# Performance work log

Hardware: AMD Instinct MI355X
Metric: run time of the kernel (lower is better)

## Reference

```python
import jax, jax.numpy as jnp
import numpy as np

N_NODES = 100000
N_EDGES = 1600000
D_FEAT = 64


def setup_inputs() -> dict:
    key = jax.random.key(0)
    k1, k2, k3 = jax.random.split(key, 3)
    adj_indices = jax.random.randint(k1, (2, N_EDGES), 0, N_NODES, dtype=jnp.int64 if jax.config.jax_enable_x64 else jnp.int32)
    # symmetric-normalized-like edge weights in (0, 1)
    adj_values = jax.random.uniform(k2, (N_EDGES,), dtype=jnp.float32)
    feats = jax.random.normal(k3, (N_NODES, D_FEAT), dtype=jnp.float32)
    return {"adj_indices": adj_indices, "adj_values": adj_values, "feats": feats}


def reference(adj_indices, adj_values, feats):
    """out = sparse_adj @ feats  (COO SpMM via gather + segment_sum).

    adj_indices: [2, E] int (row, col) coordinates of nonzeros
    adj_values : [E] float nonzero values
    feats      : [N, d] dense node features
    returns    : [N, d]
    """
    rows = adj_indices[0]
    cols = adj_indices[1]
    # gather neighbor features, scale by edge weight: [E, d]
    msgs = adj_values[:, None] * feats[cols]
    # scatter-add into destination rows: [N, d]
    return jax.ops.segment_sum(msgs, rows, num_segments=feats.shape[0])
```

## Files before the change

### kernel.cpp

```cpp
#include <hip/hip_runtime.h>

#define NN 100000
#define NE 1600000
#define DF 64
#define RPB 32
#define NBS 3328
#define NBU 3125
#define OFS_STRIDE (NBS + 1)
#define CHK 4096
#define SCAP 768
#define SPB 13

__device__ inline float bflo(unsigned int u) { return __uint_as_float(u << 16); }
__device__ inline float bfhi(unsigned int u) { return __uint_as_float(u & 0xFFFF0000u); }

__device__ inline unsigned int bfpack(float lo, float hi) {
    unsigned int ul = __float_as_uint(lo), uh = __float_as_uint(hi);
    ul = (ul + 0x7FFFu + ((ul >> 16) & 1u)) >> 16;
    uh = (uh + 0x7FFFu + ((uh >> 16) & 1u)) & 0xFFFF0000u;
    return ul | uh;
}

__global__ __launch_bounds__(256) void cvt_kernel(const float* __restrict__ feats,
                                                  uint4* __restrict__ fbf) {
    int t = blockIdx.x * blockDim.x + threadIdx.x;
    if (t >= NN * DF / 8) return;
    const float4* f4 = reinterpret_cast<const float4*>(feats);
    float4 a = f4[2 * t];
    float4 b = f4[2 * t + 1];
    uint4 o;
    o.x = bfpack(a.x, a.y);
    o.y = bfpack(a.z, a.w);
    o.z = bfpack(b.x, b.y);
    o.w = bfpack(b.z, b.w);
    fbf[t] = o;
}

__global__ __launch_bounds__(256) void part_kernel(
    const int* __restrict__ rows, const int* __restrict__ cols,
    const float* __restrict__ vals, unsigned short* __restrict__ ofs,
    int2* __restrict__ packed, int E)
{
    int c = blockIdx.x;
    int base = c * CHK;
    int n = E - base; if (n > CHK) n = CHK;
    int t = threadIdx.x;

    __shared__ int cnt[NBS];
    __shared__ int cnt2[NBS];
    __shared__ int scanv[NBS];
    __shared__ int tsum[256];

    for (int b = t; b < NBS; b += 256) { cnt[b] = 0; cnt2[b] = 0; }
    __syncthreads();

    int rr[16]; int cc[16]; float vv[16];
#pragma unroll
    for (int k = 0; k < 16; ++k) {
        int i = t + k * 256;
        if (i < n) {
            rr[k] = rows[base + i];
            cc[k] = cols[base + i];
            vv[k] = vals[base + i];
            atomicAdd(&cnt[rr[k] >> 5], 1);
        }
    }
    __syncthreads();

    int local[SPB]; int s = 0;
#pragma unroll
    for (int j = 0; j < SPB; ++j) { local[j] = cnt[t * SPB + j]; s += local[j]; }
    tsum[t] = s;
    __syncthreads();
    for (int d = 1; d < 256; d <<= 1) {
        int x = (t >= d) ? tsum[t - d] : 0;
        __syncthreads();
        tsum[t] += x;
        __syncthreads();
    }
    int run = tsum[t] - s;
#pragma unroll
    for (int j = 0; j < SPB; ++j) { scanv[t * SPB + j] = run; run += local[j]; }
    __syncthreads();

    unsigned short* og = ofs + (size_t)c * OFS_STRIDE;
    for (int b = t; b < NBS; b += 256) og[b] = (unsigned short)scanv[b];
    if (t == 0) og[NBS] = (unsigned short)n;

#pragma unroll
    for (int k = 0; k < 16; ++k) {
        int i = t + k * 256;
        if (i < n) {
            int r = rr[k];
            int b = r >> 5;
            int rank = atomicAdd(&cnt2[b], 1);
            int pos = base + scanv[b] + rank;
            packed[pos] = make_int2(cc[k] | ((r & 31) << 17), __float_as_int(vv[k]));
        }
    }
}

__global__ __launch_bounds__(256) void spmm_kernel(
    const unsigned short* __restrict__ ofs, const int2* __restrict__ packed,
    const unsigned short* __restrict__ fbf, float* __restrict__ out, int nc)
{
    int b = blockIdx.x;
    int t = threadIdx.x;

    __shared__ int2 sorted[SCAP];
    __shared__ int cnt[RPB];
    __shared__ int rstart[RPB + 1];

    if (t < RPB) cnt[t] = 0;
    __syncthreads();

    int c2 = t + 256;
    int sA = 0, eA = 0, sB = 0, eB = 0;
    if (t < nc) {
        const unsigned short* og = ofs + (size_t)t * OFS_STRIDE + b;
        sA = og[0]; eA = og[1];
    }
    if (c2 < nc) {
        const unsigned short* og = ofs + (size_t)c2 * OFS_STRIDE + b;
        sB = og[0]; eB = og[1];
    }
    int lenA = eA - sA, lenB = eB - sB;

    int2 ebA[8], ebB[8];
#pragma unroll
    for (int k = 0; k < 8; ++k) if (k < lenA) ebA[k] = packed[t * CHK + sA + k];
#pragma unroll
    for (int k = 0; k < 8; ++k) if (k < lenB) ebB[k] = packed[c2 * CHK + sB + k];

#pragma unroll
    for (int k = 0; k < 8; ++k) if (k < lenA) atomicAdd(&cnt[(ebA[k].x >> 17) & 31], 1);
    for (int i = sA + 8; i < eA; ++i) atomicAdd(&cnt[(packed[t * CHK + i].x >> 17) & 31], 1);
#pragma unroll
    for (int k = 0; k < 8; ++k) if (k < lenB) atomicAdd(&cnt[(ebB[k].x >> 17) & 31], 1);
    for (int i = sB + 8; i < eB; ++i) atomicAdd(&cnt[(packed[c2 * CHK + i].x >> 17) & 31], 1);
    __syncthreads();

    if (t < RPB) {
        int v = cnt[t];
        int incl = v;
        for (int d = 1; d < RPB; d <<= 1) {
            int x = __shfl_up(incl, d, 64);
            if (t >= d) incl += x;
        }
        rstart[t] = incl - v;
        if (t == RPB - 1) rstart[RPB] = incl;
    }
    __syncthreads();
    if (t < RPB) cnt[t] = rstart[t];
    __syncthreads();

#pragma unroll
    for (int k = 0; k < 8; ++k) if (k < lenA) {
        int rl = (ebA[k].x >> 17) & 31;
        int pos = atomicAdd(&cnt[rl], 1);
        if (pos < SCAP) sorted[pos] = make_int2(ebA[k].x & 0x1FFFF, ebA[k].y);
    }
    for (int i = sA + 8; i < eA; ++i) {
        int2 cv = packed[t * CHK + i];
        int rl = (cv.x >> 17) & 31;
        int pos = atomicAdd(&cnt[rl], 1);
        if (pos < SCAP) sorted[pos] = make_int2(cv.x & 0x1FFFF, cv.y);
    }
#pragma unroll
    for (int k = 0; k < 8; ++k) if (k < lenB) {
        int rl = (ebB[k].x >> 17) & 31;
        int pos = atomicAdd(&cnt[rl], 1);
        if (pos < SCAP) sorted[pos] = make_int2(ebB[k].x & 0x1FFFF, ebB[k].y);
    }
    for (int i = sB + 8; i < eB; ++i) {
        int2 cv = packed[c2 * CHK + i];
        int rl = (cv.x >> 17) & 31;
        int pos = atomicAdd(&cnt[rl], 1);
        if (pos < SCAP) sorted[pos] = make_int2(cv.x & 0x1FFFF, cv.y);
    }
    __syncthreads();

    int w = t >> 6;
    int lane = t & 63;
    int grp = lane >> 4;
    int fq = lane & 15;
    int rowbase = b * RPB;

    for (int rl = w * 8; rl < w * 8 + 8; ++rl) {
        int row = rowbase + rl;
        int beg = rstart[rl], end = rstart[rl + 1];
        float4 acc = make_float4(0.f, 0.f, 0.f, 0.f);
        int i = beg + grp;
        for (; i + 12 < end; i += 16) {
            int2 e0 = sorted[i];
            int2 e1 = sorted[i + 4];
            int2 e2 = sorted[i + 8];
            int2 e3 = sorted[i + 12];
            const uint2 g0 = *reinterpret_cast<const uint2*>(fbf + (size_t)e0.x * DF + fq * 4);
            const uint2 g1 = *reinterpret_cast<const uint2*>(fbf + (size_t)e1.x * DF + fq * 4);
            const uint2 g2 = *reinterpret_cast<const uint2*>(fbf + (size_t)e2.x * DF + fq * 4);
            const uint2 g3 = *reinterpret_cast<const uint2*>(fbf + (size_t)e3.x * DF + fq * 4);
            float v0 = __int_as_float(e0.y), v1 = __int_as_float(e1.y);
            float v2 = __int_as_float(e2.y), v3 = __int_as_float(e3.y);
            acc.x += v0 * bflo(g0.x); acc.y += v0 * bfhi(g0.x);
            acc.z += v0 * bflo(g0.y); acc.w += v0 * bfhi(g0.y);
            acc.x += v1 * bflo(g1.x); acc.y += v1 * bfhi(g1.x);
            acc.z += v1 * bflo(g1.y); acc.w += v1 * bfhi(g1.y);
            acc.x += v2 * bflo(g2.x); acc.y += v2 * bfhi(g2.x);
            acc.z += v2 * bflo(g2.y); acc.w += v2 * bfhi(g2.y);
            acc.x += v3 * bflo(g3.x); acc.y += v3 * bfhi(g3.x);
            acc.z += v3 * bflo(g3.y); acc.w += v3 * bfhi(g3.y);
        }
        for (; i + 4 < end; i += 8) {
            int2 e0 = sorted[i];
            int2 e1 = sorted[i + 4];
            const uint2 g0 = *reinterpret_cast<const uint2*>(fbf + (size_t)e0.x * DF + fq * 4);
            const uint2 g1 = *reinterpret_cast<const uint2*>(fbf + (size_t)e1.x * DF + fq * 4);
            float v0 = __int_as_float(e0.y), v1 = __int_as_float(e1.y);
            acc.x += v0 * bflo(g0.x); acc.y += v0 * bfhi(g0.x);
            acc.z += v0 * bflo(g0.y); acc.w += v0 * bfhi(g0.y);
            acc.x += v1 * bflo(g1.x); acc.y += v1 * bfhi(g1.x);
            acc.z += v1 * bflo(g1.y); acc.w += v1 * bfhi(g1.y);
        }
        if (i < end) {
            int2 e0 = sorted[i];
            const uint2 g0 = *reinterpret_cast<const uint2*>(fbf + (size_t)e0.x * DF + fq * 4);
            float v0 = __int_as_float(e0.y);
            acc.x += v0 * bflo(g0.x); acc.y += v0 * bfhi(g0.x);
            acc.z += v0 * bflo(g0.y); acc.w += v0 * bfhi(g0.y);
        }
#pragma unroll
        for (int m = 16; m <= 32; m <<= 1) {
            acc.x += __shfl_xor(acc.x, m, 64);
            acc.y += __shfl_xor(acc.y, m, 64);
            acc.z += __shfl_xor(acc.z, m, 64);
            acc.w += __shfl_xor(acc.w, m, 64);
        }
        if (grp == 0 && row < NN)
            *reinterpret_cast<float4*>(out + (size_t)row * DF + fq * 4) = acc;
    }
}


extern "C" void kernel_launch(void* const* d_in, const int* in_sizes, int n_in,
                              void* d_out, int out_size, void* d_ws, size_t ws_size,
                              hipStream_t stream) {
    const int* adj_indices = (const int*)d_in[0];
    const float* adj_values = (const float*)d_in[1];
    const float* feats = (const float*)d_in[2];
    float* out = (float*)d_out;

    const int E = in_sizes[1];
    const int* rows = adj_indices;
    const int* cols = adj_indices + E;

    const int nc = (E + CHK - 1) / CHK;

    unsigned short* fbf = (unsigned short*)d_ws;
    size_t fbf_bytes = (size_t)NN * DF * 2;
    unsigned short* ofs = (unsigned short*)((char*)d_ws + fbf_bytes);
    size_t ofs_bytes = (size_t)nc * OFS_STRIDE * 2;
    size_t packed_off = (fbf_bytes + ofs_bytes + 15) & ~(size_t)15;
    int2* packed = (int2*)((char*)d_ws + packed_off);

    cvt_kernel<<<(NN * DF / 8 + 255) / 256, 256, 0, stream>>>(feats, (uint4*)fbf);
    part_kernel<<<nc, 256, 0, stream>>>(rows, cols, adj_values, ofs, packed, E);
    spmm_kernel<<<NBU, 256, 0, stream>>>(ofs, packed, fbf, out, nc);
}
```

Baseline: 77.48 us.

## Flatten per-warp row loop into segmented edge stream with LDS atomic accumulation

Each wave now walks all edges of its 8 rows as one continuous stream, keeping a running per-row accumulator and flushing it into a shared-memory tile with float atomics whenever the row changes. The tile is then written to global memory with coalesced float4 stores. This removes the per-row loop overheads, tail handling and shuffle reductions, and keeps gather loads flowing across row boundaries. Block indices are also remapped so that consecutive row blocks land on the same XCD, which is meant to improve L2 locality. In exchange it adds LDS atomics, an extra 8 KB of shared memory, and a remap that hardcodes the block count.

```diff
diff --git a/kernel.cpp b/kernel.cpp
--- a/kernel.cpp
+++ b/kernel.cpp
@@ -104,14 +104,22 @@
     const unsigned short* __restrict__ ofs, const int2* __restrict__ packed,
     const unsigned short* __restrict__ fbf, float* __restrict__ out, int nc)
 {
-    int b = blockIdx.x;
+    int borig = blockIdx.x;
+    int xcd = borig & 7;
+    int sub = borig >> 3;
+    int b = (xcd < 5 ? xcd * 391 : 5 * 391 + (xcd - 5) * 390) + sub;
+
     int t = threadIdx.x;
 
     __shared__ int2 sorted[SCAP];
+    __shared__ float accs[RPB * DF];
     __shared__ int cnt[RPB];
     __shared__ int rstart[RPB + 1];
 
     if (t < RPB) cnt[t] = 0;
+#pragma unroll
+    for (int k = 0; k < 2; ++k)
+        *reinterpret_cast<float4*>(&accs[(t + k * 256) * 4]) = make_float4(0.f, 0.f, 0.f, 0.f);
     __syncthreads();
 
     int c2 = t + 256;
@@ -158,25 +166,25 @@
     for (int k = 0; k < 8; ++k) if (k < lenA) {
         int rl = (ebA[k].x >> 17) & 31;
         int pos = atomicAdd(&cnt[rl], 1);
-        if (pos < SCAP) sorted[pos] = make_int2(ebA[k].x & 0x1FFFF, ebA[k].y);
+        if (pos < SCAP) sorted[pos] = ebA[k];
     }
     for (int i = sA + 8; i < eA; ++i) {
         int2 cv = packed[t * CHK + i];
         int rl = (cv.x >> 17) & 31;
         int pos = atomicAdd(&cnt[rl], 1);
-        if (pos < SCAP) sorted[pos] = make_int2(cv.x & 0x1FFFF, cv.y);
+        if (pos < SCAP) sorted[pos] = cv;
     }
 #pragma unroll
     for (int k = 0; k < 8; ++k) if (k < lenB) {
         int rl = (ebB[k].x >> 17) & 31;
         int pos = atomicAdd(&cnt[rl], 1);
-        if (pos < SCAP) sorted[pos] = make_int2(ebB[k].x & 0x1FFFF, ebB[k].y);
+        if (pos < SCAP) sorted[pos] = ebB[k];
     }
     for (int i = sB + 8; i < eB; ++i) {
         int2 cv = packed[c2 * CHK + i];
         int rl = (cv.x >> 17) & 31;
         int pos = atomicAdd(&cnt[rl], 1);
-        if (pos < SCAP) sorted[pos] = make_int2(cv.x & 0x1FFFF, cv.y);
+        if (pos < SCAP) sorted[pos] = cv;
     }
     __syncthreads();
 
@@ -184,60 +192,105 @@
     int lane = t & 63;
     int grp = lane >> 4;
     int fq = lane & 15;
+
+    int beg = rstart[w * 8], end = rstart[w * 8 + 8];
+    float4 a4 = make_float4(0.f, 0.f, 0.f, 0.f);
+    int cur = -1;
+
+    for (int i = beg + grp; i < end; i += 16) {
+        int2 e0, e1, e2, e3;
+        uint2 g0, g1, g2, g3;
+        int j1 = i + 4, j2 = i + 8, j3 = i + 12;
+        e0 = sorted[i];
+        e1 = sorted[j1 < end ? j1 : i];
+        e2 = sorted[j2 < end ? j2 : i];
+        e3 = sorted[j3 < end ? j3 : i];
+        g0 = *reinterpret_cast<const uint2*>(fbf + (size_t)(e0.x & 0x1FFFF) * DF + fq * 4);
+        g1 = *reinterpret_cast<const uint2*>(fbf + (size_t)(e1.x & 0x1FFFF) * DF + fq * 4);
+        g2 = *reinterpret_cast<const uint2*>(fbf + (size_t)(e2.x & 0x1FFFF) * DF + fq * 4);
+        g3 = *reinterpret_cast<const uint2*>(fbf + (size_t)(e3.x & 0x1FFFF) * DF + fq * 4);
+
+        {
+            int rl = (e0.x >> 17) & 31;
+            if (rl != cur) {
+                if (cur >= 0) {
+                    atomicAdd(&accs[cur * DF + fq * 4 + 0], a4.x);
+                    atomicAdd(&accs[cur * DF + fq * 4 + 1], a4.y);
+                    atomicAdd(&accs[cur * DF + fq * 4 + 2], a4.z);
+                    atomicAdd(&accs[cur * DF + fq * 4 + 3], a4.w);
+                }
+                a4 = make_float4(0.f, 0.f, 0.f, 0.f);
+                cur = rl;
+            }
+            float v = __int_as_float(e0.y);
+            a4.x += v * bflo(g0.x); a4.y += v * bfhi(g0.x);
+            a4.z += v * bflo(g0.y); a4.w += v * bfhi(g0.y);
+        }
+        if (j1 < end) {
+            int rl = (e1.x >> 17) & 31;
+            if (rl != cur) {
+                if (cur >= 0) {
+                    atomicAdd(&accs[cur * DF + fq * 4 + 0], a4.x);
+                    atomicAdd(&accs[cur * DF + fq * 4 + 1], a4.y);
+                    atomicAdd(&accs[cur * DF + fq * 4 + 2], a4.z);
+                    atomicAdd(&accs[cur * DF + fq * 4 + 3], a4.w);
+                }
+                a4 = make_float4(0.f, 0.f, 0.f, 0.f);
+                cur = rl;
+            }
+            float v = __int_as_float(e1.y);
+            a4.x += v * bflo(g1.x); a4.y += v * bfhi(g1.x);
+            a4.z += v * bflo(g1.y); a4.w += v * bfhi(g1.y);
+        }
+        if (j2 < end) {
+            int rl = (e2.x >> 17) & 31;
+            if (rl != cur) {
+                if (cur >= 0) {
+                    atomicAdd(&accs[cur * DF + fq * 4 + 0], a4.x);
+                    atomicAdd(&accs[cur * DF + fq * 4 + 1], a4.y);
+                    atomicAdd(&accs[cur * DF + fq * 4 + 2], a4.z);
+                    atomicAdd(&accs[cur * DF + fq * 4 + 3], a4.w);
+                }
+                a4 = make_float4(0.f, 0.f, 0.f, 0.f);
+                cur = rl;
+            }
+            float v = __int_as_float(e2.y);
+            a4.x += v * bflo(g2.x); a4.y += v * bfhi(g2.x);
+            a4.z += v * bflo(g2.y); a4.w += v * bfhi(g2.y);
+        }
+        if (j3 < end) {
+            int rl = (e3.x >> 17) & 31;
+            if (rl != cur) {
+                if (cur >= 0) {
+                    atomicAdd(&accs[cur * DF + fq * 4 + 0], a4.x);
+                    atomicAdd(&accs[cur * DF + fq * 4 + 1], a4.y);
+                    atomicAdd(&accs[cur * DF + fq * 4 + 2], a4.z);
+                    atomicAdd(&accs[cur * DF + fq * 4 + 3], a4.w);
+                }
+                a4 = make_float4(0.f, 0.f, 0.f, 0.f);
+                cur = rl;
+            }
+            float v = __int_as_float(e3.y);
+            a4.x += v * bflo(g3.x); a4.y += v * bfhi(g3.x);
+            a4.z += v * bflo(g3.y); a4.w += v * bfhi(g3.y);
+        }
+    }
+    if (cur >= 0) {
+        atomicAdd(&accs[cur * DF + fq * 4 + 0], a4.x);
+        atomicAdd(&accs[cur * DF + fq * 4 + 1], a4.y);
+        atomicAdd(&accs[cur * DF + fq * 4 + 2], a4.z);
+        atomicAdd(&accs[cur * DF + fq * 4 + 3], a4.w);
+    }
+    __syncthreads();
+
     int rowbase = b * RPB;
-
-    for (int rl = w * 8; rl < w * 8 + 8; ++rl) {
-        int row = rowbase + rl;
-        int beg = rstart[rl], end = rstart[rl + 1];
-        float4 acc = make_float4(0.f, 0.f, 0.f, 0.f);
-        int i = beg + grp;
-        for (; i + 12 < end; i += 16) {
-            int2 e0 = sorted[i];
-            int2 e1 = sorted[i + 4];
-            int2 e2 = sorted[i + 8];
-            int2 e3 = sorted[i + 12];
-            const uint2 g0 = *reinterpret_cast<const uint2*>(fbf + (size_t)e0.x * DF + fq * 4);
-            const uint2 g1 = *reinterpret_cast<const uint2*>(fbf + (size_t)e1.x * DF + fq * 4);
-            const uint2 g2 = *reinterpret_cast<const uint2*>(fbf + (size_t)e2.x * DF + fq * 4);
-            const uint2 g3 = *reinterpret_cast<const uint2*>(fbf + (size_t)e3.x * DF + fq * 4);
-            float v0 = __int_as_float(e0.y), v1 = __int_as_float(e1.y);
-            float v2 = __int_as_float(e2.y), v3 = __int_as_float(e3.y);
-            acc.x += v0 * bflo(g0.x); acc.y += v0 * bfhi(g0.x);
-            acc.z += v0 * bflo(g0.y); acc.w += v0 * bfhi(g0.y);
-            acc.x += v1 * bflo(g1.x); acc.y += v1 * bfhi(g1.x);
-            acc.z += v1 * bflo(g1.y); acc.w += v1 * bfhi(g1.y);
-            acc.x += v2 * bflo(g2.x); acc.y += v2 * bfhi(g2.x);
-            acc.z += v2 * bflo(g2.y); acc.w += v2 * bfhi(g2.y);
-            acc.x += v3 * bflo(g3.x); acc.y += v3 * bfhi(g3.x);
-            acc.z += v3 * bflo(g3.y); acc.w += v3 * bfhi(g3.y);
-        }
-        for (; i + 4 < end; i += 8) {
-            int2 e0 = sorted[i];
-            int2 e1 = sorted[i + 4];
-            const uint2 g0 = *reinterpret_cast<const uint2*>(fbf + (size_t)e0.x * DF + fq * 4);
-            const uint2 g1 = *reinterpret_cast<const uint2*>(fbf + (size_t)e1.x * DF + fq * 4);
-            float v0 = __int_as_float(e0.y), v1 = __int_as_float(e1.y);
-            acc.x += v0 * bflo(g0.x); acc.y += v0 * bfhi(g0.x);
-            acc.z += v0 * bflo(g0.y); acc.w += v0 * bfhi(g0.y);
-            acc.x += v1 * bflo(g1.x); acc.y += v1 * bfhi(g1.x);
-            acc.z += v1 * bflo(g1.y); acc.w += v1 * bfhi(g1.y);
-        }
-        if (i < end) {
-            int2 e0 = sorted[i];
-            const uint2 g0 = *reinterpret_cast<const uint2*>(fbf + (size_t)e0.x * DF + fq * 4);
-            float v0 = __int_as_float(e0.y);
-            acc.x += v0 * bflo(g0.x); acc.y += v0 * bfhi(g0.x);
-            acc.z += v0 * bflo(g0.y); acc.w += v0 * bfhi(g0.y);
-        }
-#pragma unroll
-        for (int m = 16; m <= 32; m <<= 1) {
-            acc.x += __shfl_xor(acc.x, m, 64);
-            acc.y += __shfl_xor(acc.y, m, 64);
-            acc.z += __shfl_xor(acc.z, m, 64);
-            acc.w += __shfl_xor(acc.w, m, 64);
-        }
-        if (grp == 0 && row < NN)
-            *reinterpret_cast<float4*>(out + (size_t)row * DF + fq * 4) = acc;
+#pragma unroll
+    for (int k = 0; k < 2; ++k) {
+        int idx4 = t + k * 256;
+        int row = rowbase + (idx4 >> 4);
+        if (row < NN)
+            *reinterpret_cast<float4*>(out + (size_t)rowbase * DF + (size_t)idx4 * 4) =
+                *reinterpret_cast<const float4*>(&accs[idx4 * 4]);
     }
 }
 
```

After: 178.0 us. +129.7%, slower.
